# Kernel tuning notes

Hardware: AMD Instinct MI355X
Metric: run time of the kernel (lower is better)

The kernel has to match this reference:

```python
import jax, jax.numpy as jnp
import numpy as np

B, S, IN_DIM, OUT_DIM, G = 8, 2048, 512, 256, 8
CHUNK = 128  # positions per scan step; per-chunk phi = CHUNK*O*O*G floats
EPS = 1e-5   # torch LayerNorm default


def make_periods():
    # periods[i,j,g] = i*(O*G) + j*G + g + 2
    i = jnp.arange(OUT_DIM, dtype=jnp.float32)[:, None, None]
    j = jnp.arange(OUT_DIM, dtype=jnp.float32)[None, :, None]
    g = jnp.arange(G, dtype=jnp.float32)[None, None, :]
    return i * (OUT_DIM * G) + j * G + g + 2.0


def setup_inputs() -> dict:
    key = jax.random.key(0)
    ks = jax.random.split(key, 4)
    x = jax.random.normal(ks[0], (B, S, IN_DIM), dtype=jnp.float32)
    positions = jnp.arange(S, dtype=jnp.int64 if jax.config.jax_enable_x64 else jnp.int32)
    M = jax.random.uniform(ks[1], (OUT_DIM, IN_DIM), minval=-0.5, maxval=0.5, dtype=jnp.float32)
    P = jax.random.uniform(ks[2], (OUT_DIM, OUT_DIM, G), minval=-0.1, maxval=0.1, dtype=jnp.float32)
    W_res = jax.random.uniform(ks[3], (OUT_DIM, IN_DIM), minval=-0.1, maxval=0.1, dtype=jnp.float32)
    ln_scale = jnp.ones((OUT_DIM,), dtype=jnp.float32)
    ln_bias = jnp.zeros((OUT_DIM,), dtype=jnp.float32)
    periods = make_periods()
    return {"x": x, "M": M, "P": P, "W_res": W_res, "ln_scale": ln_scale,
            "ln_bias": ln_bias, "periods": periods, "positions": positions}


def layer_norm(h, scale, bias):
    mu = jnp.mean(h, axis=-1, keepdims=True)
    var = jnp.mean(jnp.square(h - mu), axis=-1, keepdims=True)  # biased, like torch
    return (h - mu) * jax.lax.rsqrt(var + EPS) * scale + bias


def reference(x, M, P, W_res, ln_scale, ln_bias, periods, positions):
    # x: (B,S,in), M: (out,in), P: (out,out,G), periods: (out,out,G)
    x_trans = layer_norm(jnp.einsum('bsi,oi->bso', x, M), ln_scale, ln_bias)

    two_pi = jnp.float32(2.0 * np.pi)
    pos_chunks = positions.astype(jnp.float32).reshape(-1, CHUNK)  # (S/CHUNK, CHUNK)

    def body(carry, pos):
        # phi: (CHUNK, O, O, G); reduce over g first to avoid the huge 5D tensor
        phi = jnp.cos(two_pi * pos[:, None, None, None] / periods)
        A = jnp.einsum('sijg,ijg->sij', phi, P)  # (CHUNK, O, O)
        return carry, A

    _, A = jax.lax.scan(body, 0, pos_chunks)
    A = A.reshape(S, OUT_DIM, OUT_DIM)  # A[s,i,j] = sum_g P[i,j,g]*cos(2*pi*k_s/T_ijg)

    Nk = jnp.einsum('bsj,sij->bsi', x_trans, A)  # (B,S,out)
    residual = jnp.einsum('bsi,oi->bso', x, W_res)  # separate residual proj
    return Nk + residual
```

## Files before the change

kernel.cpp:

```cpp
#include <hip/hip_runtime.h>
#include <hip/hip_bf16.h>
#include <math.h>

#define B_   8
#define S_   2048
#define IN_  512
#define OUT_ 256
#define G_   8


typedef float  f32x4  __attribute__((ext_vector_type(4)));
typedef short  s16x8  __attribute__((ext_vector_type(8)));
typedef __bf16 bf16x8 __attribute__((ext_vector_type(8)));
typedef unsigned short u16x8 __attribute__((ext_vector_type(8)));

__device__ __forceinline__ float cos2pi(float f) {
#if __has_builtin(__builtin_amdgcn_cosf)
    return __builtin_amdgcn_cosf(f);
#else
    return __cosf(6.28318530717958647692f * f);
#endif
}

__device__ __forceinline__ float fractf_(float f) {
#if __has_builtin(__builtin_amdgcn_fractf)
    return __builtin_amdgcn_fractf(f);
#else
    return f - floorf(f);
#endif
}

__device__ __forceinline__ unsigned short f2bf(float f) {
    unsigned u = __builtin_bit_cast(unsigned, f);
    u += 0x7fffu + ((u >> 16) & 1u);
    return (unsigned short)(u >> 16);
}

template <typename T>
__device__ __forceinline__ auto atomF_(T* p, T v, int) -> decltype(unsafeAtomicAdd(p, v)) {
    return unsafeAtomicAdd(p, v);
}
template <typename T>
__device__ __forceinline__ T atomF_(T* p, T v, long) {
    return atomicAdd(p, v);
}
__device__ __forceinline__ void atomAddF(float* p, float v) { atomF_(p, v, 0); }

template <typename T>
__device__ __forceinline__ auto mfma_bf16_(T a, T b, f32x4 c, int)
    -> decltype(__builtin_amdgcn_mfma_f32_16x16x32_bf16(a, b, c, 0, 0, 0)) {
    return __builtin_amdgcn_mfma_f32_16x16x32_bf16(a, b, c, 0, 0, 0);
}
template <typename T>
__device__ __forceinline__ auto mfma_bf16_(T a, T b, f32x4 c, long)
    -> decltype(__builtin_amdgcn_mfma_f32_16x16x32_bf16(__builtin_bit_cast(bf16x8, a),
                                                        __builtin_bit_cast(bf16x8, b), c, 0, 0, 0)) {
    return __builtin_amdgcn_mfma_f32_16x16x32_bf16(__builtin_bit_cast(bf16x8, a),
                                                   __builtin_bit_cast(bf16x8, b), c, 0, 0, 0);
}
__device__ __forceinline__ f32x4 mfma_bf16(s16x8 a, s16x8 b, f32x4 c) {
    return mfma_bf16_(a, b, c, 0);
}

__device__ __forceinline__ void gld16(const void* g, void* l) {
    __builtin_amdgcn_global_load_lds((const __attribute__((address_space(1))) unsigned int*)g,
                                     (__attribute__((address_space(3))) unsigned int*)l,
                                     16, 0, 0);
}

__device__ __forceinline__ void prep_one(const float* __restrict__ P,
                                         const float* __restrict__ periods,
                                         float4* __restrict__ PTK, int tid) {
    const int j = tid >> 8, i = tid & 255;
    float p[8], iT[8], k2[8];
#pragma unroll
    for (int g = 0; g < 8; ++g) {
        const int idx = (i * 256 + j) * 8 + g;
        p[g]  = P[idx];
        iT[g] = 1.0f / periods[idx];
        k2[g] = 2.0f * cos2pi(iT[g]);
    }
    float4* base = PTK + (size_t)(j * 6) * 256 + i;
    base[0]    = make_float4(p[0], iT[0], p[1], iT[1]);
    base[256]  = make_float4(p[2], iT[2], p[3], iT[3]);
    base[512]  = make_float4(p[4], iT[4], p[5], iT[5]);
    base[768]  = make_float4(p[6], iT[6], p[7], iT[7]);
    base[1024] = make_float4(k2[0], k2[1], k2[2], k2[3]);
    base[1280] = make_float4(k2[4], k2[5], k2[6], k2[7]);
}

__global__ __launch_bounds__(256) void cvt_prep(const float* __restrict__ x,
                                                const float* __restrict__ M,
                                                const float* __restrict__ Wres,
                                                const float* __restrict__ P,
                                                const float* __restrict__ periods,
                                                unsigned short* __restrict__ Xb,
                                                unsigned short* __restrict__ Wb,
                                                float4* __restrict__ PTK) {
    const int bid = blockIdx.x;
    if (bid >= 4224) {
        prep_one(P, periods, PTK, (bid - 4224) * 256 + threadIdx.x);
        return;
    }
    const float* src;
    unsigned short* dst;
    if (bid < 4096) {
        const int idx = bid * 256 + threadIdx.x;
        src = x + (size_t)idx * 8;
        dst = Xb + (size_t)idx * 8;
    } else {
        const int idx = (bid - 4096) * 256 + threadIdx.x;
        const int row = idx >> 6;
        const int col = (idx & 63) * 8;
        src = (row < 256) ? (M + (size_t)row * 512 + col)
                          : (Wres + (size_t)(row - 256) * 512 + col);
        dst = Wb + (size_t)row * 512 + col;
    }
    const float4 v0 = *(const float4*)(src);
    const float4 v1 = *(const float4*)(src + 4);
    u16x8 o;
    o[0] = f2bf(v0.x); o[1] = f2bf(v0.y); o[2] = f2bf(v0.z); o[3] = f2bf(v0.w);
    o[4] = f2bf(v1.x); o[5] = f2bf(v1.y); o[6] = f2bf(v1.z); o[7] = f2bf(v1.w);
    *(u16x8*)dst = o;
}

__global__ __launch_bounds__(256) void cvt_xw(const float* __restrict__ x,
                                              const float* __restrict__ M,
                                              const float* __restrict__ Wres,
                                              unsigned short* __restrict__ Xb,
                                              unsigned short* __restrict__ Wb) {
    const int bid = blockIdx.x;
    const float* src;
    unsigned short* dst;
    if (bid < 4096) {
        const int idx = bid * 256 + threadIdx.x;
        src = x + (size_t)idx * 8;
        dst = Xb + (size_t)idx * 8;
    } else {
        const int idx = (bid - 4096) * 256 + threadIdx.x;
        const int row = idx >> 6;
        const int col = (idx & 63) * 8;
        src = (row < 256) ? (M + (size_t)row * 512 + col)
                          : (Wres + (size_t)(row - 256) * 512 + col);
        dst = Wb + (size_t)row * 512 + col;
    }
    const float4 v0 = *(const float4*)(src);
    const float4 v1 = *(const float4*)(src + 4);
    u16x8 o;
    o[0] = f2bf(v0.x); o[1] = f2bf(v0.y); o[2] = f2bf(v0.z); o[3] = f2bf(v0.w);
    o[4] = f2bf(v1.x); o[5] = f2bf(v1.y); o[6] = f2bf(v1.z); o[7] = f2bf(v1.w);
    *(u16x8*)dst = o;
}

__global__ __launch_bounds__(256) void prep_ptk(const float* __restrict__ P,
                                                const float* __restrict__ periods,
                                                float4* __restrict__ PTK) {
    prep_one(P, periods, PTK, blockIdx.x * 256 + threadIdx.x);
}

__global__ __launch_bounds__(256) void gemm_mfma(const unsigned short* __restrict__ Xb,
                                                 const unsigned short* __restrict__ Wb,
                                                 float* __restrict__ y,
                                                 float* __restrict__ out) {
    __shared__ __align__(16) unsigned short At[64 * 64];
    __shared__ __align__(16) unsigned short Bt[128 * 64];
    const int t    = threadIdx.x;
    const int col0 = blockIdx.x * 128;
    const int row0 = blockIdx.y * 64;

    const unsigned short* ga[2]; int la[2];
    const unsigned short* gb[4]; int lb[4];
#pragma unroll
    for (int cc = 0; cc < 2; ++cc) {
        const int L = cc * 256 + t;
        const int r = L >> 3;
        const int c = (L & 7) ^ (r & 7);
        ga[cc] = Xb + (size_t)(row0 + r) * 512 + c * 8;
        la[cc] = L * 8;
    }
#pragma unroll
    for (int cc = 0; cc < 4; ++cc) {
        const int L = cc * 256 + t;
        const int r = L >> 3;
        const int c = (L & 7) ^ (r & 7);
        gb[cc] = Wb + (size_t)(col0 + r) * 512 + c * 8;
        lb[cc] = L * 8;
    }

    const int lane = t & 63;
    const int wave = t >> 6;
    const int wn   = wave * 32;
    const int quad = lane >> 4;
    const int l16  = lane & 15;

    f32x4 acc[4][2];
#pragma unroll
    for (int mi = 0; mi < 4; ++mi)
#pragma unroll
        for (int ni = 0; ni < 2; ++ni) acc[mi][ni] = {0.0f, 0.0f, 0.0f, 0.0f};

    for (int k0 = 0; k0 < 512; k0 += 64) {
        __syncthreads();
#pragma unroll
        for (int cc = 0; cc < 2; ++cc) gld16(ga[cc] + k0, At + la[cc]);
#pragma unroll
        for (int cc = 0; cc < 4; ++cc) gld16(gb[cc] + k0, Bt + lb[cc]);
        __syncthreads();
#pragma unroll
        for (int ks = 0; ks < 2; ++ks) {
            const int cc = (ks * 4 + quad) ^ (l16 & 7);
            s16x8 af[4], bf[2];
#pragma unroll
            for (int mi = 0; mi < 4; ++mi) {
                const int ra = mi * 16 + l16;
                af[mi] = *(const s16x8*)(At + (ra * 8 + cc) * 8);
            }
#pragma unroll
            for (int ni = 0; ni < 2; ++ni) {
                const int rb = wn + ni * 16 + l16;
                bf[ni] = *(const s16x8*)(Bt + (rb * 8 + cc) * 8);
            }
#pragma unroll
            for (int mi = 0; mi < 4; ++mi)
#pragma unroll
                for (int ni = 0; ni < 2; ++ni)
                    acc[mi][ni] = mfma_bf16(af[mi], bf[ni], acc[mi][ni]);
        }
    }

    float* dst   = (col0 < 256) ? y : out;
    const int cb = (col0 & 255) + wn;
#pragma unroll
    for (int mi = 0; mi < 4; ++mi) {
        const int rbase = row0 + mi * 16 + quad * 4;
#pragma unroll
        for (int ni = 0; ni < 2; ++ni) {
            const int col = cb + ni * 16 + l16;
#pragma unroll
            for (int rg = 0; rg < 4; ++rg)
                dst[(size_t)(rbase + rg) * 256 + col] = acc[mi][ni][rg];
        }
    }
}

__global__ __launch_bounds__(256) void gemm_kernel(const float* __restrict__ x,
                                                   const float* __restrict__ M,
                                                   const float* __restrict__ Wres,
                                                   float* __restrict__ y,
                                                   float* __restrict__ out) {
    __shared__ float As[8][132];
    __shared__ float Bs[8][132];
    const int ct = blockIdx.x;
    const int rt = blockIdx.y;
    const int t  = threadIdx.x;
    const int row0 = rt * 128;
    const float* W = (ct < 2) ? M : Wres;
    const int wcol0 = (ct & 1) * 128;
    float acc[8][8];
#pragma unroll
    for (int r = 0; r < 8; ++r)
#pragma unroll
        for (int c = 0; c < 8; ++c) acc[r][c] = 0.0f;
    const int lr = t >> 1;
    const int lk = (t & 1) << 2;
    for (int k0 = 0; k0 < 512; k0 += 8) {
        float4 av = *(const float4*)(x + (size_t)(row0 + lr) * 512 + k0 + lk);
        float4 bv = *(const float4*)(W + (size_t)(wcol0 + lr) * 512 + k0 + lk);
        __syncthreads();
        As[lk + 0][lr] = av.x; As[lk + 1][lr] = av.y; As[lk + 2][lr] = av.z; As[lk + 3][lr] = av.w;
        Bs[lk + 0][lr] = bv.x; Bs[lk + 1][lr] = bv.y; Bs[lk + 2][lr] = bv.z; Bs[lk + 3][lr] = bv.w;
        __syncthreads();
        const int tx = t & 15, ty = t >> 4;
#pragma unroll
        for (int kk = 0; kk < 8; ++kk) {
            const float4 a0 = *(const float4*)&As[kk][ty * 8];
            const float4 a1 = *(const float4*)&As[kk][ty * 8 + 4];
            const float4 b0 = *(const float4*)&Bs[kk][tx * 8];
            const float4 b1 = *(const float4*)&Bs[kk][tx * 8 + 4];
            const float ar[8] = {a0.x, a0.y, a0.z, a0.w, a1.x, a1.y, a1.z, a1.w};
            const float br[8] = {b0.x, b0.y, b0.z, b0.w, b1.x, b1.y, b1.z, b1.w};
#pragma unroll
            for (int r = 0; r < 8; ++r)
#pragma unroll
                for (int c = 0; c < 8; ++c) acc[r][c] = fmaf(ar[r], br[c], acc[r][c]);
        }
    }
    const int tx = t & 15, ty = t >> 4;
    float* dst = (ct < 2) ? y : out;
    const int cbase = (ct & 1) * 128 + tx * 8;
#pragma unroll
    for (int r = 0; r < 8; ++r) {
        float4 v0 = {acc[r][0], acc[r][1], acc[r][2], acc[r][3]};
        float4 v1 = {acc[r][4], acc[r][5], acc[r][6], acc[r][7]};
        float* p = dst + (size_t)(row0 + ty * 8 + r) * 256 + cbase;
        *(float4*)(p)     = v0;
        *(float4*)(p + 4) = v1;
    }
}

__global__ __launch_bounds__(256, 4) void cosnk_lnjs(const float4* __restrict__ PTK,
                                                     const float* __restrict__ ypre,
                                                     const float* __restrict__ ln_scale,
                                                     const float* __restrict__ ln_bias,
                                                     float* __restrict__ out) {
    __shared__ float xs[128 * 64];
    const int t  = threadIdx.x;
    const int bx = blockIdx.x;
    const int ih = (bx >> 2) & 1;
    const int rid = ((bx >> 3) << 2) | (bx & 3);
    const int stile = rid >> 1;
    const int jh = rid & 1;
    const int s0 = stile * 8;
    const int jbase = jh * 128;

    {
        const int slot = t >> 2;
        const int st   = slot >> 3;
        const int b    = slot & 7;
        const int jg   = t & 3;
        const float* src = ypre + (size_t)(b * S_ + s0 + st) * 256 + jg * 64;
        float4 v[16];
        float sum = 0.0f, ssq = 0.0f;
#pragma unroll
        for (int q = 0; q < 16; ++q) {
            v[q] = *(const float4*)(src + 4 * q);
            sum += v[q].x + v[q].y + v[q].z + v[q].w;
            ssq += v[q].x * v[q].x + v[q].y * v[q].y + v[q].z * v[q].z + v[q].w * v[q].w;
        }
        sum += __shfl_xor(sum, 1); sum += __shfl_xor(sum, 2);
        ssq += __shfl_xor(ssq, 1); ssq += __shfl_xor(ssq, 2);
        const float mu  = sum * (1.0f / 256.0f);
        const float var = ssq * (1.0f / 256.0f) - mu * mu;
        const float rs  = rsqrtf(var + 1e-5f);
        if ((jg >> 1) == jh) {
            const int jl0s = (jg & 1) * 64;
#pragma unroll
            for (int q = 0; q < 16; ++q) {
                const float4 sc = *(const float4*)(ln_scale + jg * 64 + 4 * q);
                const float4 bi = *(const float4*)(ln_bias  + jg * 64 + 4 * q);
                const int jl = jl0s + 4 * q;
                xs[(jl + 0) * 64 + slot] = (v[q].x - mu) * rs * sc.x + bi.x;
                xs[(jl + 1) * 64 + slot] = (v[q].y - mu) * rs * sc.y + bi.y;
                xs[(jl + 2) * 64 + slot] = (v[q].z - mu) * rs * sc.z + bi.z;
                xs[(jl + 3) * 64 + slot] = (v[q].w - mu) * rs * sc.w + bi.w;
            }
        }
    }
    __syncthreads();

    const int i   = ih * 128 + (t & 127);
    const int jq  = t >> 7;
    const int jl0 = jq * 64;
    const float sv0 = (float)s0;

    float acc[8][8];
#pragma unroll
    for (int s = 0; s < 8; ++s)
#pragma unroll
        for (int b = 0; b < 8; ++b) acc[s][b] = 0.0f;

    const float4* ptk = PTK + (size_t)(jbase + jl0) * 1536 + i;
    float4 q0 = ptk[0],    q1 = ptk[256],  q2 = ptk[512];
    float4 q3 = ptk[768], k01 = ptk[1024], k23 = ptk[1280];

#define CHEB8(p_, iT_, k2_)                         \
    do {                                            \
        float f0 = fractf_(sv0 * (iT_));            \
        float c0 = cos2pi(f0);                      \
        float c1 = cos2pi(fractf_(f0 + (iT_)));     \
        float c2 = fmaf((k2_), c1, -c0);            \
        float c3 = fmaf((k2_), c2, -c1);            \
        float c4 = fmaf((k2_), c3, -c2);            \
        float c5 = fmaf((k2_), c4, -c3);            \
        float c6 = fmaf((k2_), c5, -c4);            \
        float c7 = fmaf((k2_), c6, -c5);            \
        a0 = fmaf((p_), c0, a0); a1 = fmaf((p_), c1, a1); \
        a2 = fmaf((p_), c2, a2); a3 = fmaf((p_), c3, a3); \
        a4 = fmaf((p_), c4, a4); a5 = fmaf((p_), c5, a5); \
        a6 = fmaf((p_), c6, a6); a7 = fmaf((p_), c7, a7); \
    } while (0)

    for (int jj = 0; jj < 64; ++jj) {
        const float4* pn = ptk + ((jj < 63) ? 1536 : 0);
        const float4 n0 = pn[0],   n1 = pn[256],  n2 = pn[512];
        const float4 n3 = pn[768], n4 = pn[1024], n5 = pn[1280];

        float a0 = 0.f, a1 = 0.f, a2 = 0.f, a3 = 0.f, a4 = 0.f, a5 = 0.f, a6 = 0.f, a7 = 0.f;
        CHEB8(q0.x, q0.y, k01.x);
        CHEB8(q0.z, q0.w, k01.y);
        CHEB8(q1.x, q1.y, k01.z);
        CHEB8(q1.z, q1.w, k01.w);
        CHEB8(q2.x, q2.y, k23.x);
        CHEB8(q2.z, q2.w, k23.y);
        CHEB8(q3.x, q3.y, k23.z);
        CHEB8(q3.z, q3.w, k23.w);

        const float* xrow = &xs[(jl0 + jj) * 64];
        const float as_[8] = {a0, a1, a2, a3, a4, a5, a6, a7};
#pragma unroll
        for (int s = 0; s < 8; ++s) {
            const float4 xa = *(const float4*)(xrow + s * 8);
            const float4 xb = *(const float4*)(xrow + s * 8 + 4);
            acc[s][0] = fmaf(as_[s], xa.x, acc[s][0]);
            acc[s][1] = fmaf(as_[s], xa.y, acc[s][1]);
            acc[s][2] = fmaf(as_[s], xa.z, acc[s][2]);
            acc[s][3] = fmaf(as_[s], xa.w, acc[s][3]);
            acc[s][4] = fmaf(as_[s], xb.x, acc[s][4]);
            acc[s][5] = fmaf(as_[s], xb.y, acc[s][5]);
            acc[s][6] = fmaf(as_[s], xb.z, acc[s][6]);
            acc[s][7] = fmaf(as_[s], xb.w, acc[s][7]);
        }
        q0 = n0; q1 = n1; q2 = n2; q3 = n3; k01 = n4; k23 = n5;
        ptk = pn;
    }
#undef CHEB8

    __syncthreads();
    const int tl = t & 127;
    if (jq) {
#pragma unroll
        for (int slot = 0; slot < 64; ++slot)
            xs[slot * 128 + tl] = acc[slot >> 3][slot & 7];
    }
    __syncthreads();
    if (!jq) {
#pragma unroll
        for (int slot = 0; slot < 64; ++slot) {
            const int st = slot >> 3, b = slot & 7;
            const float v = acc[st][b] + xs[slot * 128 + tl];
            atomAddF(&out[(size_t)(b * S_ + s0 + st) * 256 + i], v);
        }
    }
}

extern "C" void kernel_launch(void* const* d_in, const int* in_sizes, int n_in,
                              void* d_out, int out_size, void* d_ws, size_t ws_size,
                              hipStream_t stream) {
    const float* x        = (const float*)d_in[0];
    const float* M        = (const float*)d_in[1];
    const float* P        = (const float*)d_in[2];
    const float* Wres     = (const float*)d_in[3];
    const float* ln_scale = (const float*)d_in[4];
    const float* ln_bias  = (const float*)d_in[5];
    const float* periods  = (const float*)d_in[6];

    float* out = (float*)d_out;
    char*  wsb = (char*)d_ws;
    const size_t MB = 1024 * 1024;
    float* y = (float*)wsb;
    unsigned short* Xb = (unsigned short*)(wsb + 16 * MB);
    unsigned short* Wb = (unsigned short*)(wsb + 32 * MB);

    const bool big  = (ws_size >= 39 * MB);
    const bool mfma = (ws_size >= (size_t)34078720);

    float4* PTK;
    if (big) {
        PTK = (float4*)(wsb + 33 * MB);
        cvt_prep<<<4480, 256, 0, stream>>>(x, M, Wres, P, periods, Xb, Wb, PTK);
        dim3 ggrid(4, 256);
        gemm_mfma<<<ggrid, 256, 0, stream>>>(Xb, Wb, y, out);
    } else if (mfma) {
        PTK = (float4*)(wsb + 16 * MB);
        cvt_xw<<<4224, 256, 0, stream>>>(x, M, Wres, Xb, Wb);
        dim3 ggrid(4, 256);
        gemm_mfma<<<ggrid, 256, 0, stream>>>(Xb, Wb, y, out);
        prep_ptk<<<256, 256, 0, stream>>>(P, periods, PTK);
    } else {
        PTK = (float4*)(wsb + 16 * MB);
        dim3 ggrid(4, 128);
        gemm_kernel<<<ggrid, 256, 0, stream>>>(x, M, Wres, y, out);
        prep_ptk<<<256, 256, 0, stream>>>(P, periods, PTK);
    }

    cosnk_lnjs<<<1024, 256, 0, stream>>>(PTK, y, ln_scale, ln_bias, out);
}
```

Before: 244.5 us.

## Vectorize Chebyshev cosine recurrence with packed float2 math and split out LayerNorm

The main cos/Chebyshev accumulation loop is rewritten to use 2-wide float vectors, so the compiler can emit packed FP32 instructions (v_pk_fma/v_pk_mul) for both the recurrence and the outer-product accumulation. To make that work, the PTK layout changes so P, 1/T and k2 are stored contiguously per group. LayerNorm moves out of the main kernel into a separate in-place pass over y, which removes the redundant per-block LN recomputation but adds a kernel launch and one extra read/write of y.

```diff
diff --git a/kernel.cpp b/kernel.cpp
--- a/kernel.cpp
+++ b/kernel.cpp
@@ -9,6 +9,7 @@
 #define G_   8
 
 
+typedef float  f32x2  __attribute__((ext_vector_type(2)));
 typedef float  f32x4  __attribute__((ext_vector_type(4)));
 typedef short  s16x8  __attribute__((ext_vector_type(8)));
 typedef __bf16 bf16x8 __attribute__((ext_vector_type(8)));
@@ -68,6 +69,9 @@
                                      16, 0, 0);
 }
 
+__device__ __forceinline__ f32x2 lo2(float4 v) { f32x2 r; r.x = v.x; r.y = v.y; return r; }
+__device__ __forceinline__ f32x2 hi2(float4 v) { f32x2 r; r.x = v.z; r.y = v.w; return r; }
+
 __device__ __forceinline__ void prep_one(const float* __restrict__ P,
                                          const float* __restrict__ periods,
                                          float4* __restrict__ PTK, int tid) {
@@ -81,10 +85,10 @@
         k2[g] = 2.0f * cos2pi(iT[g]);
     }
     float4* base = PTK + (size_t)(j * 6) * 256 + i;
-    base[0]    = make_float4(p[0], iT[0], p[1], iT[1]);
-    base[256]  = make_float4(p[2], iT[2], p[3], iT[3]);
-    base[512]  = make_float4(p[4], iT[4], p[5], iT[5]);
-    base[768]  = make_float4(p[6], iT[6], p[7], iT[7]);
+    base[0]    = make_float4(p[0],  p[1],  p[2],  p[3]);
+    base[256]  = make_float4(p[4],  p[5],  p[6],  p[7]);
+    base[512]  = make_float4(iT[0], iT[1], iT[2], iT[3]);
+    base[768]  = make_float4(iT[4], iT[5], iT[6], iT[7]);
     base[1024] = make_float4(k2[0], k2[1], k2[2], k2[3]);
     base[1280] = make_float4(k2[4], k2[5], k2[6], k2[7]);
 }
@@ -298,11 +302,37 @@
     }
 }
 
-__global__ __launch_bounds__(256, 4) void cosnk_lnjs(const float4* __restrict__ PTK,
-                                                     const float* __restrict__ ypre,
-                                                     const float* __restrict__ ln_scale,
-                                                     const float* __restrict__ ln_bias,
-                                                     float* __restrict__ out) {
+__global__ __launch_bounds__(256) void ln_kernel(float* __restrict__ y,
+                                                 const float* __restrict__ scale,
+                                                 const float* __restrict__ bias) {
+    const int t    = threadIdx.x;
+    const int row  = blockIdx.x * 4 + (t >> 6);
+    const int lane = t & 63;
+    float* p = y + (size_t)row * 256 + lane * 4;
+    float4 v = *(float4*)p;
+    float s  = v.x + v.y + v.z + v.w;
+    float ss = v.x * v.x + v.y * v.y + v.z * v.z + v.w * v.w;
+#pragma unroll
+    for (int off = 32; off > 0; off >>= 1) {
+        s  += __shfl_xor(s, off);
+        ss += __shfl_xor(ss, off);
+    }
+    const float mu  = s * (1.0f / 256.0f);
+    const float var = ss * (1.0f / 256.0f) - mu * mu;
+    const float rs  = rsqrtf(var + 1e-5f);
+    float4 sc = *(const float4*)(scale + lane * 4);
+    float4 bi = *(const float4*)(bias + lane * 4);
+    float4 o;
+    o.x = (v.x - mu) * rs * sc.x + bi.x;
+    o.y = (v.y - mu) * rs * sc.y + bi.y;
+    o.z = (v.z - mu) * rs * sc.z + bi.z;
+    o.w = (v.w - mu) * rs * sc.w + bi.w;
+    *(float4*)p = o;
+}
+
+__global__ __launch_bounds__(256, 4) void cosnk_pk(const float4* __restrict__ PTK,
+                                                   const float* __restrict__ xt,
+                                                   float* __restrict__ out) {
     __shared__ float xs[128 * 64];
     const int t  = threadIdx.x;
     const int bx = blockIdx.x;
@@ -318,32 +348,15 @@
         const int st   = slot >> 3;
         const int b    = slot & 7;
         const int jg   = t & 3;
-        const float* src = ypre + (size_t)(b * S_ + s0 + st) * 256 + jg * 64;
-        float4 v[16];
-        float sum = 0.0f, ssq = 0.0f;
-#pragma unroll
-        for (int q = 0; q < 16; ++q) {
-            v[q] = *(const float4*)(src + 4 * q);
-            sum += v[q].x + v[q].y + v[q].z + v[q].w;
-            ssq += v[q].x * v[q].x + v[q].y * v[q].y + v[q].z * v[q].z + v[q].w * v[q].w;
-        }
-        sum += __shfl_xor(sum, 1); sum += __shfl_xor(sum, 2);
-        ssq += __shfl_xor(ssq, 1); ssq += __shfl_xor(ssq, 2);
-        const float mu  = sum * (1.0f / 256.0f);
-        const float var = ssq * (1.0f / 256.0f) - mu * mu;
-        const float rs  = rsqrtf(var + 1e-5f);
-        if ((jg >> 1) == jh) {
-            const int jl0s = (jg & 1) * 64;
-#pragma unroll
-            for (int q = 0; q < 16; ++q) {
-                const float4 sc = *(const float4*)(ln_scale + jg * 64 + 4 * q);
-                const float4 bi = *(const float4*)(ln_bias  + jg * 64 + 4 * q);
-                const int jl = jl0s + 4 * q;
-                xs[(jl + 0) * 64 + slot] = (v[q].x - mu) * rs * sc.x + bi.x;
-                xs[(jl + 1) * 64 + slot] = (v[q].y - mu) * rs * sc.y + bi.y;
-                xs[(jl + 2) * 64 + slot] = (v[q].z - mu) * rs * sc.z + bi.z;
-                xs[(jl + 3) * 64 + slot] = (v[q].w - mu) * rs * sc.w + bi.w;
-            }
+        const float* src = xt + (size_t)(b * S_ + s0 + st) * 256 + jbase + jg * 32;
+#pragma unroll
+        for (int q = 0; q < 8; ++q) {
+            float4 v = *(const float4*)(src + 4 * q);
+            const int jl = jg * 32 + 4 * q;
+            xs[(jl + 0) * 64 + slot] = v.x;
+            xs[(jl + 1) * 64 + slot] = v.y;
+            xs[(jl + 2) * 64 + slot] = v.z;
+            xs[(jl + 3) * 64 + slot] = v.w;
         }
     }
     __syncthreads();
@@ -352,32 +365,37 @@
     const int jq  = t >> 7;
     const int jl0 = jq * 64;
     const float sv0 = (float)s0;
-
-    float acc[8][8];
+    f32x2 sv0v; sv0v.x = sv0; sv0v.y = sv0;
+
+    f32x2 accP[8][4];
 #pragma unroll
     for (int s = 0; s < 8; ++s)
 #pragma unroll
-        for (int b = 0; b < 8; ++b) acc[s][b] = 0.0f;
+        for (int q = 0; q < 4; ++q) { accP[s][q].x = 0.0f; accP[s][q].y = 0.0f; }
 
     const float4* ptk = PTK + (size_t)(jbase + jl0) * 1536 + i;
-    float4 q0 = ptk[0],    q1 = ptk[256],  q2 = ptk[512];
-    float4 q3 = ptk[768], k01 = ptk[1024], k23 = ptk[1280];
-
-#define CHEB8(p_, iT_, k2_)                         \
-    do {                                            \
-        float f0 = fractf_(sv0 * (iT_));            \
-        float c0 = cos2pi(f0);                      \
-        float c1 = cos2pi(fractf_(f0 + (iT_)));     \
-        float c2 = fmaf((k2_), c1, -c0);            \
-        float c3 = fmaf((k2_), c2, -c1);            \
-        float c4 = fmaf((k2_), c3, -c2);            \
-        float c5 = fmaf((k2_), c4, -c3);            \
-        float c6 = fmaf((k2_), c5, -c4);            \
-        float c7 = fmaf((k2_), c6, -c5);            \
-        a0 = fmaf((p_), c0, a0); a1 = fmaf((p_), c1, a1); \
-        a2 = fmaf((p_), c2, a2); a3 = fmaf((p_), c3, a3); \
-        a4 = fmaf((p_), c4, a4); a5 = fmaf((p_), c5, a5); \
-        a6 = fmaf((p_), c6, a6); a7 = fmaf((p_), c7, a7); \
+    float4 qp0 = ptk[0],    qp1 = ptk[256];
+    float4 qt0 = ptk[512],  qt1 = ptk[768];
+    float4 qk0 = ptk[1024], qk1 = ptk[1280];
+
+#define CHEBP(p2_, t2_, k2_)                                \
+    do {                                                    \
+        f32x2 f0 = sv0v * (t2_);                            \
+        f0.x = fractf_(f0.x); f0.y = fractf_(f0.y);         \
+        f32x2 c0; c0.x = cos2pi(f0.x); c0.y = cos2pi(f0.y); \
+        f32x2 f1 = f0 + (t2_);                              \
+        f1.x = fractf_(f1.x); f1.y = fractf_(f1.y);         \
+        f32x2 c1; c1.x = cos2pi(f1.x); c1.y = cos2pi(f1.y); \
+        f32x2 c2 = (k2_) * c1 - c0;                         \
+        f32x2 c3 = (k2_) * c2 - c1;                         \
+        f32x2 c4 = (k2_) * c3 - c2;                         \
+        f32x2 c5 = (k2_) * c4 - c3;                         \
+        f32x2 c6 = (k2_) * c5 - c4;                         \
+        f32x2 c7 = (k2_) * c6 - c5;                         \
+        A0 += (p2_) * c0; A1 += (p2_) * c1;                 \
+        A2 += (p2_) * c2; A3 += (p2_) * c3;                 \
+        A4 += (p2_) * c4; A5 += (p2_) * c5;                 \
+        A6 += (p2_) * c6; A7 += (p2_) * c7;                 \
     } while (0)
 
     for (int jj = 0; jj < 64; ++jj) {
@@ -385,49 +403,47 @@
         const float4 n0 = pn[0],   n1 = pn[256],  n2 = pn[512];
         const float4 n3 = pn[768], n4 = pn[1024], n5 = pn[1280];
 
-        float a0 = 0.f, a1 = 0.f, a2 = 0.f, a3 = 0.f, a4 = 0.f, a5 = 0.f, a6 = 0.f, a7 = 0.f;
-        CHEB8(q0.x, q0.y, k01.x);
-        CHEB8(q0.z, q0.w, k01.y);
-        CHEB8(q1.x, q1.y, k01.z);
-        CHEB8(q1.z, q1.w, k01.w);
-        CHEB8(q2.x, q2.y, k23.x);
-        CHEB8(q2.z, q2.w, k23.y);
-        CHEB8(q3.x, q3.y, k23.z);
-        CHEB8(q3.z, q3.w, k23.w);
+        f32x2 A0 = {0.f, 0.f}, A1 = {0.f, 0.f}, A2 = {0.f, 0.f}, A3 = {0.f, 0.f};
+        f32x2 A4 = {0.f, 0.f}, A5 = {0.f, 0.f}, A6 = {0.f, 0.f}, A7 = {0.f, 0.f};
+        CHEBP(lo2(qp0), lo2(qt0), lo2(qk0));
+        CHEBP(hi2(qp0), hi2(qt0), hi2(qk0));
+        CHEBP(lo2(qp1), lo2(qt1), lo2(qk1));
+        CHEBP(hi2(qp1), hi2(qt1), hi2(qk1));
+
+        const float as_[8] = {A0.x + A0.y, A1.x + A1.y, A2.x + A2.y, A3.x + A3.y,
+                              A4.x + A4.y, A5.x + A5.y, A6.x + A6.y, A7.x + A7.y};
 
         const float* xrow = &xs[(jl0 + jj) * 64];
-        const float as_[8] = {a0, a1, a2, a3, a4, a5, a6, a7};
 #pragma unroll
         for (int s = 0; s < 8; ++s) {
             const float4 xa = *(const float4*)(xrow + s * 8);
             const float4 xb = *(const float4*)(xrow + s * 8 + 4);
-            acc[s][0] = fmaf(as_[s], xa.x, acc[s][0]);
-            acc[s][1] = fmaf(as_[s], xa.y, acc[s][1]);
-            acc[s][2] = fmaf(as_[s], xa.z, acc[s][2]);
-            acc[s][3] = fmaf(as_[s], xa.w, acc[s][3]);
-            acc[s][4] = fmaf(as_[s], xb.x, acc[s][4]);
-            acc[s][5] = fmaf(as_[s], xb.y, acc[s][5]);
-            acc[s][6] = fmaf(as_[s], xb.z, acc[s][6]);
-            acc[s][7] = fmaf(as_[s], xb.w, acc[s][7]);
-        }
-        q0 = n0; q1 = n1; q2 = n2; q3 = n3; k01 = n4; k23 = n5;
+            f32x2 av; av.x = as_[s]; av.y = as_[s];
+            accP[s][0] += av * lo2(xa);
+            accP[s][1] += av * hi2(xa);
+            accP[s][2] += av * lo2(xb);
+            accP[s][3] += av * hi2(xb);
+        }
+        qp0 = n0; qp1 = n1; qt0 = n2; qt1 = n3; qk0 = n4; qk1 = n5;
         ptk = pn;
     }
-#undef CHEB8
+#undef CHEBP
 
     __syncthreads();
     const int tl = t & 127;
     if (jq) {
 #pragma unroll
-        for (int slot = 0; slot < 64; ++slot)
-            xs[slot * 128 + tl] = acc[slot >> 3][slot & 7];
+        for (int slot = 0; slot < 64; ++slot) {
+            const int st = slot >> 3, b = slot & 7;
+            xs[slot * 128 + tl] = accP[st][b >> 1][b & 1];
+        }
     }
     __syncthreads();
     if (!jq) {
 #pragma unroll
         for (int slot = 0; slot < 64; ++slot) {
             const int st = slot >> 3, b = slot & 7;
-            const float v = acc[st][b] + xs[slot * 128 + tl];
+            const float v = accP[st][b >> 1][b & 1] + xs[slot * 128 + tl];
             atomAddF(&out[(size_t)(b * S_ + s0 + st) * 256 + i], v);
         }
     }
@@ -473,5 +489,7 @@
         prep_ptk<<<256, 256, 0, stream>>>(P, periods, PTK);
     }
 
-    cosnk_lnjs<<<1024, 256, 0, stream>>>(PTK, y, ln_scale, ln_bias, out);
-}
+    ln_kernel<<<4096, 256, 0, stream>>>(y, ln_scale, ln_bias);
+
+    cosnk_pk<<<1024, 256, 0, stream>>>(PTK, y, out);
+}
```

Result: faster. 234.4 us (-4.1%).
